# Kernel optimization log

Measured on AMD Instinct MI355X. Metric: run time of the kernel, lower is better.

## Reference

```python
import jax, jax.numpy as jnp
import numpy as np

H, SK, SV, PK, PV = 12, 16, 16, 4, 8
SCALAR_DIM, PAIR_DIM = 384, 128
SIZES = [SK*H, SK*H, SV*H, PK*H*3, PK*H*3, PV*H*3]  # qkv split sizes
N_LOGITS = 3
SS = (N_LOGITS * SK) ** -0.5                 # scalar logit scale
PS = (N_LOGITS * PK * 4.5) ** -0.5           # point logit scale
PBS = N_LOGITS ** -0.5                       # pair bias scale
EPS = 1e-8


def setup_inputs() -> dict:
    key = jax.random.key(0)
    ks = jax.random.split(key, 16)
    b, n = 1, 768
    scalar_feats = jax.random.normal(ks[0], (b, n, SCALAR_DIM), jnp.float32)
    pair_feats = jax.random.normal(ks[1], (b, n, n, PAIR_DIM), jnp.float32)
    rotations = jax.random.normal(ks[2], (b, n, 3, 3), jnp.float32)
    translations = jax.random.normal(ks[3], (b, n, 3), jnp.float32)
    mask = jnp.ones((b, n), dtype=bool)
    d_qkv = sum(SIZES)
    sc = SCALAR_DIM ** -0.5
    Wqkv = jax.random.normal(ks[4], (SCALAR_DIM, d_qkv), jnp.float32) * sc
    Wpb = jax.random.normal(ks[5], (PAIR_DIM, H), jnp.float32) * PAIR_DIM ** -0.5
    point_weights = jnp.full((1, H, 1, 1), float(np.log(np.e - 1.0)), jnp.float32)
    dim_out = H * (PAIR_DIM + SV + 4 * PV)  # 2112
    Wout = jax.random.normal(ks[6], (dim_out, SCALAR_DIM), jnp.float32) * dim_out ** -0.5
    bout = jnp.zeros((SCALAR_DIM,), jnp.float32)
    Wp1 = jax.random.normal(ks[7], (3 * H, PAIR_DIM), jnp.float32) * (3 * H) ** -0.5
    bp1 = jnp.zeros((PAIR_DIM,), jnp.float32)
    Wp2 = jax.random.normal(ks[8], (PAIR_DIM, PAIR_DIM), jnp.float32) * PAIR_DIM ** -0.5
    bp2 = jnp.zeros((PAIR_DIM,), jnp.float32)
    return dict(scalar_feats=scalar_feats, pair_feats=pair_feats, rotations=rotations,
                translations=translations, mask=mask, Wqkv=Wqkv, Wpb=Wpb,
                point_weights=point_weights, Wout=Wout, bout=bout,
                Wp1=Wp1, bp1=bp1, Wp2=Wp2, bp2=bp2)


def _heads(x, b, n, d):
    # b n (h d) -> b h n d
    return x.reshape(b, n, H, d).transpose(0, 2, 1, 3)


def _merge(x):
    # b h n d -> b n (h d)
    b, h, n, d = x.shape
    return x.transpose(0, 2, 1, 3).reshape(b, n, h * d)


def ipa_forward(scalar_feats, pair_feats, rotations, translations, mask,
                Wqkv, Wpb, point_weights, Wout, bout, Wp1, bp1, Wp2, bp2):
    b, n, _ = scalar_feats.shape
    qkv = scalar_feats @ Wqkv
    offs = np.cumsum([0] + SIZES)
    qs, ks_, vs, qp, kp, vp = [qkv[..., offs[i]:offs[i + 1]] for i in range(6)]
    qs, ks_, vs = _heads(qs, b, n, SK), _heads(ks_, b, n, SK), _heads(vs, b, n, SV)

    def to_global_points(p, d):
        p = p.reshape(b, n, H * d, 3)                       # ... (d c) -> ... d c
        p = jnp.einsum('bixy,bidy->bidx', rotations, p) + translations[:, :, None, :]
        return p.reshape(b, n, H, d, 3).transpose(0, 2, 1, 3, 4)  # b h n d 3

    qp, kp = to_global_points(qp, PK), to_global_points(kp, PK)
    vp = to_global_points(vp, PV)

    scalar_logits = jnp.einsum('bhid,bhjd->bhij', qs, ks_)
    pair_bias = jnp.einsum('bijd,dh->bhij', pair_feats, Wpb)
    point_logits = jnp.einsum('bhidc,bhjdc->bhij', qp, kp) * jax.nn.softplus(point_weights)

    m2 = mask[:, None, :, None] & mask[:, None, None, :]    # b 1 i j
    neg = -jnp.finfo(scalar_logits.dtype).max
    scalar_logits = jnp.where(m2, scalar_logits, neg)
    point_logits = jnp.where(m2, point_logits, neg)
    pair_bias = jnp.where(m2, pair_bias, neg)

    attn = jax.nn.softmax(SS * scalar_logits + PS * point_logits + PBS * pair_bias, axis=-1)

    res_scalar = jnp.einsum('bhij,bhjd->bhid', attn, vs)
    res_pair = jnp.einsum('bhij,bijd->bhid', attn, pair_feats)
    res_pts = jnp.einsum('bhij,bhjdc->bhidc', attn, vp)
    # inverse rigid: R^T (p - t)
    local = jnp.einsum('biyx,bhidy->bhidx', rotations,
                       res_pts - translations[:, None, :, None, :])
    pts_norm = jnp.sqrt(jnp.sum(local ** 2, axis=-1) + EPS)  # safe_norm

    feats = jnp.concatenate([
        _merge(res_scalar),                                   # b n h*SV
        _merge(res_pair),                                     # b n h*PAIR_DIM
        _merge(local.reshape(b, H, n, PV * 3)),               # b n h*PV*3
        _merge(pts_norm),                                     # b n h*PV
    ], axis=-1)
    scalar_out = feats @ Wout + bout

    edge = jnp.concatenate([attn,
                            jax.nn.softmax(point_logits, axis=-1),
                            jax.nn.softmax(scalar_logits, axis=-1)], axis=1)
    edge = edge.transpose(0, 2, 3, 1)                         # b i j (3h)
    pair_out = jax.nn.gelu(edge @ Wp1 + bp1, approximate=False) @ Wp2 + bp2
    return scalar_out, pair_out


def reference(scalar_feats, pair_feats, rotations, translations, mask,
              Wqkv, Wpb, point_weights, Wout, bout, Wp1, bp1, Wp2, bp2):
    return ipa_forward(scalar_feats, pair_feats, rotations, translations, mask,
                       Wqkv, Wpb, point_weights, Wout, bout, Wp1, bp1, Wp2, bp2)
```

## Files before the change

### kernel.cpp

```cpp
#include <hip/hip_runtime.h>
#include <hip/hip_bf16.h>
#include <math.h>

#define NRES 768
#define NH 12
#define DQKV 1152
#define PAIRD 128
#define SCD 384
#define DOUTF 2112

#define SS_C 0.14433756729740643f
#define PS_C 0.13608276348795434f
#define PBS_C 0.5773502691896258f

typedef __attribute__((ext_vector_type(4))) float f32x4;
typedef __attribute__((ext_vector_type(8))) short s16x8;

__device__ __forceinline__ unsigned short f2bf(float x) {
  union { float f; unsigned u; } v; v.f = x;
  unsigned r = (v.u + 0x7fffu + ((v.u >> 16) & 1u)) >> 16;
  return (unsigned short)r;
}
__device__ __forceinline__ float bf2f(unsigned short h) {
  union { unsigned u; float f; } v; v.u = (unsigned)h << 16;
  return v.f;
}

__device__ __forceinline__ float gelu_f(float x) {
  float z = x * 0.70710678118654752f;
  float az = fabsf(z);
  float t = __builtin_amdgcn_rcpf(1.f + 0.3275911f * az);
  float poly = t * (0.254829592f + t * (-0.284496736f +
               t * (1.421413741f + t * (-1.453152027f + t * 1.061405429f))));
  float e = __expf(-az * az);
  float erfv = 1.f - poly * e;
  erfv = (z < 0.f) ? -erfv : erfv;
  return 0.5f * x * (1.f + erfv);
}

__global__ __launch_bounds__(256) void gemm_bf16(
    const unsigned short* __restrict__ A, const unsigned short* __restrict__ Bt,
    const float* __restrict__ bias, float* __restrict__ C,
    int M, int Nn, int K)
{
  __shared__ __align__(16) unsigned short A_lds[64][72];
  __shared__ __align__(16) unsigned short B_lds[64][72];
  int m0 = blockIdx.y * 64, n0 = blockIdx.x * 64;
  int t = threadIdx.x;
  int lane = t & 63, w = t >> 6;
  int n15 = lane & 15, q = lane >> 4;
  f32x4 acc[4];
#pragma unroll
  for (int nt = 0; nt < 4; ++nt) acc[nt] = (f32x4){0.f, 0.f, 0.f, 0.f};
  for (int k0 = 0; k0 < K; k0 += 64) {
    __syncthreads();
#pragma unroll
    for (int u = 0; u < 2; ++u) {
      int idx = t + u * 256;
      int r = idx >> 3, c = (idx & 7) * 8;
      *(s16x8*)&A_lds[r][c] = *(const s16x8*)&A[(size_t)(m0 + r) * K + k0 + c];
      *(s16x8*)&B_lds[r][c] = *(const s16x8*)&Bt[(size_t)(n0 + r) * K + k0 + c];
    }
    __syncthreads();
#pragma unroll
    for (int ks = 0; ks < 2; ++ks) {
      s16x8 af = *(const s16x8*)&A_lds[w * 16 + n15][ks * 32 + q * 8];
#pragma unroll
      for (int nt = 0; nt < 4; ++nt) {
        s16x8 bf = *(const s16x8*)&B_lds[nt * 16 + n15][ks * 32 + q * 8];
        acc[nt] = __builtin_amdgcn_mfma_f32_16x16x32_bf16(af, bf, acc[nt], 0, 0, 0);
      }
    }
  }
#pragma unroll
  for (int nt = 0; nt < 4; ++nt) {
    int n = n0 + nt * 16 + n15;
    float bv = bias ? bias[n] : 0.f;
#pragma unroll
    for (int r = 0; r < 4; ++r) {
      int m = m0 + w * 16 + q * 4 + r;
      C[(size_t)m * Nn + n] = acc[nt][r] + bv;
    }
  }
}

__global__ __launch_bounds__(256) void prep_wqkv_kernel(
    const float* __restrict__ W, unsigned short* __restrict__ Bt)
{
  __shared__ float tile[32][33];
  int k0 = blockIdx.x * 32, n0 = blockIdx.y * 32;
  int t = threadIdx.x;
  int x = t & 31, y = t >> 5;
#pragma unroll
  for (int r = 0; r < 32; r += 8)
    tile[y + r][x] = W[(size_t)(k0 + y + r) * DQKV + n0 + x];
  __syncthreads();
#pragma unroll
  for (int r = 0; r < 32; r += 8) {
    float v = tile[x][y + r];
    unsigned short hi = f2bf(v);
    unsigned short lo = f2bf(v - bf2f(hi));
    size_t nrow = (size_t)(n0 + y + r) * 1152;
    Bt[nrow + k0 + x]       = hi;
    Bt[nrow + 384 + k0 + x] = lo;
    Bt[nrow + 768 + k0 + x] = hi;
  }
}

__global__ __launch_bounds__(128) void prep_a_kernel(
    const float* __restrict__ A, unsigned short* __restrict__ Ap)
{
  int i = blockIdx.x, t = threadIdx.x;
#pragma unroll
  for (int p = 0; p < 3; ++p) {
    int c = t + p * 128;
    float v = A[(size_t)i * SCD + c];
    unsigned short hi = f2bf(v);
    unsigned short lo = f2bf(v - bf2f(hi));
    size_t row = (size_t)i * 1152;
    Ap[row + c]       = hi;
    Ap[row + 384 + c] = hi;
    Ap[row + 768 + c] = lo;
  }
}

__global__ __launch_bounds__(256) void wt_kernel(
    const float* __restrict__ W, unsigned short* __restrict__ Wt)
{
  __shared__ float tile[32][33];
  int k0 = blockIdx.x * 32, n0 = blockIdx.y * 32;
  int t = threadIdx.x;
  int x = t & 31, y = t >> 5;
#pragma unroll
  for (int r = 0; r < 32; r += 8)
    tile[y + r][x] = W[(size_t)(k0 + y + r) * SCD + n0 + x];
  __syncthreads();
#pragma unroll
  for (int r = 0; r < 32; r += 8)
    Wt[(size_t)(n0 + y + r) * DOUTF + k0 + x] = f2bf(tile[x][y + r]);
}

__global__ __launch_bounds__(192) void points_kernel(
    const float* __restrict__ qkv, const float* __restrict__ rot,
    const float* __restrict__ trans, float* __restrict__ QP,
    float* __restrict__ KP, float* __restrict__ VP, float* __restrict__ Kq)
{
  int i = blockIdx.x;
  int t = threadIdx.x;
  const float* R = rot + (size_t)i * 9;
  const float* T = trans + (size_t)i * 3;
  int base; float* outp;
  if (t < 48) { int h = t >> 2, d = t & 3; base = 576 + (h * 4 + d) * 3;
    outp = QP + ((size_t)h * NRES + i) * 12 + d * 3; }
  else if (t < 96) { int u = t - 48; int h = u >> 2, d = u & 3; base = 720 + (h * 4 + d) * 3;
    outp = KP + ((size_t)h * NRES + i) * 12 + d * 3; }
  else { int u = t - 96; int h = u >> 3, d = u & 7; base = 864 + (h * 8 + d) * 3;
    outp = VP + ((size_t)h * NRES + i) * 24 + d * 3; }
  const float* p = qkv + (size_t)i * DQKV + base;
  float p0 = p[0], p1 = p[1], p2 = p[2];
#pragma unroll
  for (int x = 0; x < 3; ++x)
    outp[x] = R[x * 3 + 0] * p0 + R[x * 3 + 1] * p1 + R[x * 3 + 2] * p2 + T[x];
  {
    int h = t >> 4, d = t & 15;
    Kq[((size_t)h * NRES + i) * 16 + d] = qkv[(size_t)i * DQKV + 192 + h * 16 + d];
  }
}

__global__ __launch_bounds__(256) void vt_kernel(
    const float* __restrict__ qkv, const float* __restrict__ VP,
    unsigned short* __restrict__ Vt)
{
  int b = blockIdx.x;
  int h = b / 48, o = b % 48;
  int t = threadIdx.x;
  for (int p = 0; p < 3; ++p) {
    int j = p * 256 + t;
    float v;
    if (o < 16) v = qkv[(size_t)j * DQKV + 384 + h * 16 + o];
    else if (o < 40) v = VP[((size_t)h * NRES + j) * 24 + (o - 16)];
    else v = 0.f;
    Vt[((size_t)h * 48 + o) * NRES + j] = f2bf(v);
  }
}

__global__ __launch_bounds__(256) void pair_bias_kernel(
    const float* __restrict__ pair, const float* __restrict__ Wpb,
    float* __restrict__ Lb, unsigned short* __restrict__ pair_bT)
{
  __shared__ __align__(16) unsigned short Bt[64][136];
  int jt = blockIdx.x, i = blockIdx.y;
  int j0 = jt * 64;
  int t = threadIdx.x;
  int lane = t & 63, w = t >> 6;
  int n15 = lane & 15, q = lane >> 4;
  s16x8 wf[4];
#pragma unroll
  for (int ks = 0; ks < 4; ++ks) {
#pragma unroll
    for (int jj = 0; jj < 8; ++jj) {
      int k = ks * 32 + q * 8 + jj;
      float v = (n15 < 12) ? Wpb[k * 12 + n15] : 0.f;
      wf[ks][jj] = (short)f2bf(v);
    }
  }
  {
    int dq = t & 31, jb = t >> 5;
    for (int p = 0; p < 8; ++p) {
      int j = p * 8 + jb;
      float4 v = *(const float4*)(pair + ((size_t)i * NRES + j0 + j) * PAIRD + dq * 4);
      unsigned lo = (unsigned)f2bf(v.x) | ((unsigned)f2bf(v.y) << 16);
      unsigned hi = (unsigned)f2bf(v.z) | ((unsigned)f2bf(v.w) << 16);
      uint2 pk; pk.x = lo; pk.y = hi;
      *(uint2*)&Bt[j][dq * 4] = pk;
    }
  }
  __syncthreads();
  f32x4 acc = {0.f, 0.f, 0.f, 0.f};
  int m = w * 16 + n15;
#pragma unroll
  for (int ks = 0; ks < 4; ++ks) {
    s16x8 af = *(const s16x8*)&Bt[m][ks * 32 + q * 8];
    acc = __builtin_amdgcn_mfma_f32_16x16x32_bf16(af, wf[ks], acc, 0, 0, 0);
  }
  if (n15 < 12) {
    int j = j0 + w * 16 + q * 4;
    float4 st; st.x = acc[0]; st.y = acc[1]; st.z = acc[2]; st.w = acc[3];
    *(float4*)(Lb + ((size_t)n15 * NRES + i) * NRES + j) = st;
  }
  {
    int d = t >> 1, jh = t & 1;
#pragma unroll
    for (int c = 0; c < 4; ++c) {
      s16x8 pk;
#pragma unroll
      for (int e = 0; e < 8; ++e)
        pk[e] = (short)Bt[jh * 32 + c * 8 + e][d];
      *(s16x8*)&pair_bT[((size_t)i * PAIRD + d) * NRES + j0 + jh * 32 + c * 8] = pk;
    }
  }
}

#define RL 4
__global__ __launch_bounds__(256) void logits_softmax_kernel(
    const float* __restrict__ qkv, const float* __restrict__ Kq,
    const float* __restrict__ QP, const float* __restrict__ KP,
    const float* __restrict__ pw, const float* __restrict__ Lb,
    unsigned short* __restrict__ attn_b, unsigned short* __restrict__ sp_b,
    unsigned short* __restrict__ ss_b)
{
  int it = blockIdx.x, h = blockIdx.y;
  int i0 = it * RL;
  int t = threadIdx.x;
  __shared__ float q_sh[RL][28];
  if (t < RL * 28) {
    int r = t / 28, c = t % 28;
    q_sh[r][c] = (c < 16) ? qkv[(size_t)(i0 + r) * DQKV + h * 16 + c]
                          : QP[((size_t)h * NRES + i0 + r) * 12 + (c - 16)];
  }
  __syncthreads();
  float spw = log1pf(expf(pw[h]));
  float s[RL][3], p[RL][3], c[RL][3];
#pragma unroll
  for (int e = 0; e < 3; ++e) {
    int j = t + e * 256;
    float kr[16];
    const float* kq = Kq + ((size_t)h * NRES + j) * 16;
    *(float4*)&kr[0]  = *(const float4*)(kq + 0);
    *(float4*)&kr[4]  = *(const float4*)(kq + 4);
    *(float4*)&kr[8]  = *(const float4*)(kq + 8);
    *(float4*)&kr[12] = *(const float4*)(kq + 12);
    float kp[12];
    const float* kpp = KP + ((size_t)h * NRES + j) * 12;
    *(float4*)&kp[0] = *(const float4*)(kpp + 0);
    *(float4*)&kp[4] = *(const float4*)(kpp + 4);
    *(float4*)&kp[8] = *(const float4*)(kpp + 8);
#pragma unroll
    for (int r = 0; r < RL; ++r) {
      float sv = 0.f;
#pragma unroll
      for (int d = 0; d < 16; ++d) sv += q_sh[r][d] * kr[d];
      float pv = 0.f;
#pragma unroll
      for (int d = 0; d < 12; ++d) pv += q_sh[r][16 + d] * kp[d];
      pv *= spw;
      float bv = Lb[((size_t)h * NRES + i0 + r) * NRES + j];
      s[r][e] = sv; p[r][e] = pv;
      c[r][e] = SS_C * sv + PS_C * pv + PBS_C * bv;
    }
  }
  __shared__ float redm[4][RL][3];
  __shared__ float redsu[4][RL][3];
  int wv = t >> 6;
#pragma unroll
  for (int r = 0; r < RL; ++r) {
    float ms = fmaxf(fmaxf(s[r][0], s[r][1]), s[r][2]);
    float mp = fmaxf(fmaxf(p[r][0], p[r][1]), p[r][2]);
    float mc = fmaxf(fmaxf(c[r][0], c[r][1]), c[r][2]);
#pragma unroll
    for (int o = 32; o > 0; o >>= 1) {
      ms = fmaxf(ms, __shfl_down(ms, o));
      mp = fmaxf(mp, __shfl_down(mp, o));
      mc = fmaxf(mc, __shfl_down(mc, o));
    }
    if ((t & 63) == 0) { redm[wv][r][0] = ms; redm[wv][r][1] = mp; redm[wv][r][2] = mc; }
  }
  __syncthreads();
  float Ms[RL], Mp[RL], Mc[RL];
#pragma unroll
  for (int r = 0; r < RL; ++r) {
    Ms[r] = fmaxf(fmaxf(redm[0][r][0], redm[1][r][0]), fmaxf(redm[2][r][0], redm[3][r][0]));
    Mp[r] = fmaxf(fmaxf(redm[0][r][1], redm[1][r][1]), fmaxf(redm[2][r][1], redm[3][r][1]));
    Mc[r] = fmaxf(fmaxf(redm[0][r][2], redm[1][r][2]), fmaxf(redm[2][r][2], redm[3][r][2]));
  }
#pragma unroll
  for (int r = 0; r < RL; ++r) {
    float sums = 0.f, sump = 0.f, sumc = 0.f;
#pragma unroll
    for (int e = 0; e < 3; ++e) {
      float es = __expf(s[r][e] - Ms[r]); s[r][e] = es; sums += es;
      float ep = __expf(p[r][e] - Mp[r]); p[r][e] = ep; sump += ep;
      float ec = __expf(c[r][e] - Mc[r]); c[r][e] = ec; sumc += ec;
    }
#pragma unroll
    for (int o = 32; o > 0; o >>= 1) {
      sums += __shfl_down(sums, o);
      sump += __shfl_down(sump, o);
      sumc += __shfl_down(sumc, o);
    }
    if ((t & 63) == 0) { redsu[wv][r][0] = sums; redsu[wv][r][1] = sump; redsu[wv][r][2] = sumc; }
  }
  __syncthreads();
#pragma unroll
  for (int r = 0; r < RL; ++r) {
    float rs = 1.f / (redsu[0][r][0] + redsu[1][r][0] + redsu[2][r][0] + redsu[3][r][0]);
    float rp = 1.f / (redsu[0][r][1] + redsu[1][r][1] + redsu[2][r][1] + redsu[3][r][1]);
    float rc = 1.f / (redsu[0][r][2] + redsu[1][r][2] + redsu[2][r][2] + redsu[3][r][2]);
    size_t off = ((size_t)h * NRES + i0 + r) * NRES;
#pragma unroll
    for (int e = 0; e < 3; ++e) {
      int j = t + e * 256;
      ss_b[off + j]   = f2bf(s[r][e] * rs);
      sp_b[off + j]   = f2bf(p[r][e] * rp);
      attn_b[off + j] = f2bf(c[r][e] * rc);
    }
  }
}

__global__ __launch_bounds__(192) void res_sv_kernel(
    const unsigned short* __restrict__ attn, const unsigned short* __restrict__ Vt,
    float* __restrict__ res_sv)
{
  __shared__ __align__(16) unsigned short A_lds[16][72];
  __shared__ __align__(16) unsigned short B_lds[48][72];
  int it = blockIdx.x, h = blockIdx.y;
  int i0 = it * 16;
  int t = threadIdx.x;
  int lane = t & 63, w = t >> 6;
  int n15 = lane & 15, q = lane >> 4;
  f32x4 acc = {0.f, 0.f, 0.f, 0.f};
  for (int jt = 0; jt < 12; ++jt) {
    int j0 = jt * 64;
    __syncthreads();
    for (int idx = t; idx < 512; idx += 192) {
      int r = idx >> 5, j2 = idx & 31;
      *(unsigned*)&A_lds[r][j2 * 2] =
          *(const unsigned*)&attn[((size_t)h * NRES + i0 + r) * NRES + j0 + j2 * 2];
    }
    for (int idx = t; idx < 1536; idx += 192) {
      int o = idx >> 5, j2 = idx & 31;
      *(unsigned*)&B_lds[o][j2 * 2] =
          *(const unsigned*)&Vt[((size_t)h * 48 + o) * NRES + j0 + j2 * 2];
    }
    __syncthreads();
#pragma unroll
    for (int ks = 0; ks < 2; ++ks) {
      s16x8 af = *(const s16x8*)&A_lds[n15][ks * 32 + q * 8];
      s16x8 bf = *(const s16x8*)&B_lds[w * 16 + n15][ks * 32 + q * 8];
      acc = __builtin_amdgcn_mfma_f32_16x16x32_bf16(af, bf, acc, 0, 0, 0);
    }
  }
  int o = w * 16 + n15;
  if (o < 40) {
#pragma unroll
    for (int r = 0; r < 4; ++r) {
      int i = i0 + q * 4 + r;
      res_sv[((size_t)h * NRES + i) * 40 + o] = acc[r];
    }
  }
}

__global__ __launch_bounds__(256) void res_pair_kernel(
    const unsigned short* __restrict__ attn, const unsigned short* __restrict__ pair_bT,
    float* __restrict__ res_pair)
{
  __shared__ __align__(16) unsigned short A_lds[16][72];
  __shared__ __align__(16) unsigned short B_lds[128][72];
  int i = blockIdx.x;
  int t = threadIdx.x;
  int lane = t & 63, w = t >> 6;
  int n15 = lane & 15, q = lane >> 4;
  for (int idx = t; idx < 4 * 72; idx += 256)
    A_lds[12 + idx / 72][idx % 72] = 0;
  f32x4 acc[2];
  acc[0] = (f32x4){0.f, 0.f, 0.f, 0.f};
  acc[1] = (f32x4){0.f, 0.f, 0.f, 0.f};
  for (int jt = 0; jt < 12; ++jt) {
    int j0 = jt * 64;
    __syncthreads();
    for (int idx = t; idx < 384; idx += 256) {
      int r = idx >> 5, j2 = idx & 31;
      *(unsigned*)&A_lds[r][j2 * 2] =
          *(const unsigned*)&attn[((size_t)r * NRES + i) * NRES + j0 + j2 * 2];
    }
#pragma unroll
    for (int p = 0; p < 4; ++p) {
      int chunk = t + p * 256;
      int d = chunk >> 3, jc = (chunk & 7) * 8;
      *(s16x8*)&B_lds[d][jc] =
          *(const s16x8*)&pair_bT[((size_t)i * PAIRD + d) * NRES + j0 + jc];
    }
    __syncthreads();
#pragma unroll
    for (int ks = 0; ks < 2; ++ks) {
      s16x8 af = *(const s16x8*)&A_lds[n15][ks * 32 + q * 8];
#pragma unroll
      for (int nt = 0; nt < 2; ++nt) {
        int o = (w * 2 + nt) * 16 + n15;
        s16x8 bf = *(const s16x8*)&B_lds[o][ks * 32 + q * 8];
        acc[nt] = __builtin_amdgcn_mfma_f32_16x16x32_bf16(af, bf, acc[nt], 0, 0, 0);
      }
    }
  }
#pragma unroll
  for (int nt = 0; nt < 2; ++nt) {
    int o = (w * 2 + nt) * 16 + n15;
#pragma unroll
    for (int r = 0; r < 4; ++r) {
      int hh = q * 4 + r;
      if (hh < 12)
        res_pair[((size_t)hh * NRES + i) * PAIRD + o] = acc[nt][r];
    }
  }
}

__global__ __launch_bounds__(256) void feats_kernel(
    const float* __restrict__ res_sv, const float* __restrict__ res_pair,
    const float* __restrict__ rot, const float* __restrict__ trans,
    unsigned short* __restrict__ feats)
{
  int i = blockIdx.x;
  int t = threadIdx.x;
  unsigned short* F = feats + (size_t)i * DOUTF;
  if (t < 192) {
    int h = t >> 4, d = t & 15;
    F[t] = f2bf(res_sv[((size_t)h * NRES + i) * 40 + d]);
  }
  for (int e = 0; e < 6; ++e) {
    int idx = e * 256 + t;
    int h = idx >> 7, o = idx & 127;
    F[192 + idx] = f2bf(res_pair[((size_t)h * NRES + i) * PAIRD + o]);
  }
  if (t < 96) {
    int h = t >> 3, d = t & 7;
    const float* R = rot + (size_t)i * 9;
    const float* T = trans + (size_t)i * 3;
    const float* pp = res_sv + ((size_t)h * NRES + i) * 40 + 16 + d * 3;
    float p0 = pp[0] - T[0], p1 = pp[1] - T[1], p2 = pp[2] - T[2];
    float l0 = R[0] * p0 + R[3] * p1 + R[6] * p2;
    float l1 = R[1] * p0 + R[4] * p1 + R[7] * p2;
    float l2 = R[2] * p0 + R[5] * p1 + R[8] * p2;
    F[1728 + h * 24 + d * 3 + 0] = f2bf(l0);
    F[1728 + h * 24 + d * 3 + 1] = f2bf(l1);
    F[1728 + h * 24 + d * 3 + 2] = f2bf(l2);
    F[2016 + h * 8 + d] = f2bf(sqrtf(l0 * l0 + l1 * l1 + l2 * l2 + 1e-8f));
  }
}

__global__ __launch_bounds__(256) void mlp_kernel(
    const unsigned short* __restrict__ attn, const unsigned short* __restrict__ sp,
    const unsigned short* __restrict__ ss, const float* __restrict__ Wp1,
    const float* __restrict__ bp1, const float* __restrict__ Wp2,
    const float* __restrict__ bp2, float* __restrict__ out)
{
  __shared__ __align__(16) unsigned short E_lds[2][64][72];
  __shared__ __align__(16) unsigned short A_lds[64][136];
  int t = threadIdx.x;
  int lane = t & 63, w = t >> 6;
  int n15 = lane & 15, q = lane >> 4;
  for (int idx = t; idx < 64 * 28 * 2; idx += 256) {
    int b = idx / (64 * 28);
    int r = (idx / 28) % 64, k = 36 + idx % 28;
    E_lds[b][r][k] = 0;
  }
  s16x8 w1f[2][2], w2f[4][2];
#pragma unroll
  for (int ks = 0; ks < 2; ++ks)
#pragma unroll
    for (int nt = 0; nt < 2; ++nt) {
      int nn = (w * 2 + nt) * 16 + n15;
#pragma unroll
      for (int jj = 0; jj < 8; ++jj) {
        int k = ks * 32 + q * 8 + jj;
        w1f[ks][nt][jj] = (k < 36) ? (short)f2bf(Wp1[(size_t)k * 128 + nn]) : (short)0;
      }
    }
#pragma unroll
  for (int ks = 0; ks < 4; ++ks)
#pragma unroll
    for (int nt = 0; nt < 2; ++nt) {
      int nn = (w * 2 + nt) * 16 + n15;
#pragma unroll
      for (int jj = 0; jj < 8; ++jj) {
        int k = ks * 32 + q * 8 + jj;
        w2f[ks][nt][jj] = (short)f2bf(Wp2[(size_t)k * 128 + nn]);
      }
    }
  float b1v[2], b2v[2];
#pragma unroll
  for (int nt = 0; nt < 2; ++nt) {
    int nn = (w * 2 + nt) * 16 + n15;
    b1v[nt] = bp1[nn];
    b2v[nt] = bp2[nn];
  }
  const unsigned short* bufs[3] = {attn, sp, ss};
  const int NT = NRES * 12;
  int ej = t & 63, ecb = t >> 6;
  int tile = blockIdx.x;
  int cur = 0;
  if (tile < NT) {
    int i = tile / 12, j0 = (tile % 12) * 64;
#pragma unroll
    for (int p = 0; p < 9; ++p) {
      int cc = ecb * 9 + p;
      E_lds[0][ej][cc] = bufs[cc / 12][((size_t)(cc % 12) * NRES + i) * NRES + j0 + ej];
    }
  }
  for (; tile < NT; tile += gridDim.x) {
    int nxt = tile + gridDim.x;
    __syncthreads();
    unsigned short ev[9];
    if (nxt < NT) {
      int i2 = nxt / 12, j02 = (nxt % 12) * 64;
#pragma unroll
      for (int p = 0; p < 9; ++p) {
        int cc = ecb * 9 + p;
        ev[p] = bufs[cc / 12][((size_t)(cc % 12) * NRES + i2) * NRES + j02 + ej];
      }
    }
    f32x4 c1[4][2];
#pragma unroll
    for (int mt = 0; mt < 4; ++mt) {
#pragma unroll
      for (int nt = 0; nt < 2; ++nt) c1[mt][nt] = (f32x4){0.f, 0.f, 0.f, 0.f};
#pragma unroll
      for (int ks = 0; ks < 2; ++ks) {
        s16x8 af = *(const s16x8*)&E_lds[cur][mt * 16 + n15][ks * 32 + q * 8];
#pragma unroll
        for (int nt = 0; nt < 2; ++nt)
          c1[mt][nt] = __builtin_amdgcn_mfma_f32_16x16x32_bf16(af, w1f[ks][nt], c1[mt][nt], 0, 0, 0);
      }
    }
#pragma unroll
    for (int mt = 0; mt < 4; ++mt)
#pragma unroll
      for (int nt = 0; nt < 2; ++nt) {
        int o = (w * 2 + nt) * 16 + n15;
#pragma unroll
        for (int r = 0; r < 4; ++r) {
          float x = c1[mt][nt][r] + b1v[nt];
          A_lds[mt * 16 + q * 4 + r][o] = f2bf(gelu_f(x));
        }
      }
    if (nxt < NT) {
#pragma unroll
      for (int p = 0; p < 9; ++p)
        E_lds[cur ^ 1][ej][ecb * 9 + p] = ev[p];
    }
    __syncthreads();
    int i = tile / 12, j0 = (tile % 12) * 64;
    f32x4 c2[4][2];
#pragma unroll
    for (int mt = 0; mt < 4; ++mt) {
#pragma unroll
      for (int nt = 0; nt < 2; ++nt) c2[mt][nt] = (f32x4){0.f, 0.f, 0.f, 0.f};
#pragma unroll
      for (int ks = 0; ks < 4; ++ks) {
        s16x8 af = *(const s16x8*)&A_lds[mt * 16 + n15][ks * 32 + q * 8];
#pragma unroll
        for (int nt = 0; nt < 2; ++nt)
          c2[mt][nt] = __builtin_amdgcn_mfma_f32_16x16x32_bf16(af, w2f[ks][nt], c2[mt][nt], 0, 0, 0);
      }
    }
#pragma unroll
    for (int mt = 0; mt < 4; ++mt)
#pragma unroll
      for (int nt = 0; nt < 2; ++nt) {
        int o = (w * 2 + nt) * 16 + n15;
        int jb = j0 + mt * 16 + q * 4;
#pragma unroll
        for (int r = 0; r < 4; ++r)
          out[((size_t)i * NRES + jb + r) * PAIRD + o] = c2[mt][nt][r] + b2v[nt];
      }
    cur ^= 1;
  }
}

extern "C" void kernel_launch(void* const* d_in, const int* in_sizes, int n_in,
                              void* d_out, int out_size, void* d_ws, size_t ws_size,
                              hipStream_t stream) {
  const float* scalar_feats = (const float*)d_in[0];
  const float* pair  = (const float*)d_in[1];
  const float* rot   = (const float*)d_in[2];
  const float* trans = (const float*)d_in[3];
  const float* Wqkv  = (const float*)d_in[5];
  const float* Wpb   = (const float*)d_in[6];
  const float* pw    = (const float*)d_in[7];
  const float* Wout  = (const float*)d_in[8];
  const float* bout  = (const float*)d_in[9];
  const float* Wp1   = (const float*)d_in[10];
  const float* bp1   = (const float*)d_in[11];
  const float* Wp2   = (const float*)d_in[12];
  const float* bp2   = (const float*)d_in[13];
  float* out = (float*)d_out;
  float* ws = (float*)d_ws;

  float* qkv = ws;
  float* QP  = ws + 884736;
  float* KP  = ws + 995328;
  float* VP  = ws + 1105920;
  unsigned short* Vt = (unsigned short*)(ws + 1327104);
  float* Lb  = ws + 1548288;
  unsigned short* attn_b = (unsigned short*)(ws + 8626176);
  unsigned short* sp_b   = (unsigned short*)(ws + 12165120);
  unsigned short* ss_b   = (unsigned short*)(ws + 15704064);
  float* res_sv   = ws + 19243008;
  float* res_pair = ws + 19611648;
  unsigned short* feats_b = (unsigned short*)(ws + 20791296);
  unsigned short* Wout_t  = (unsigned short*)(ws + 21602304);
  float* Kq = ws + 22007808;
  unsigned short* Aprime  = (unsigned short*)(ws + 22155264);
  unsigned short* Wqkv_t  = (unsigned short*)(ws + 22597632);
  unsigned short* pair_bT = (unsigned short*)(ws + 23261184);

  prep_wqkv_kernel<<<dim3(SCD / 32, DQKV / 32), 256, 0, stream>>>(Wqkv, Wqkv_t);
  prep_a_kernel<<<NRES, 128, 0, stream>>>(scalar_feats, Aprime);
  gemm_bf16<<<dim3(DQKV / 64, NRES / 64), 256, 0, stream>>>(
      Aprime, Wqkv_t, nullptr, qkv, NRES, DQKV, 1152);
  points_kernel<<<NRES, 192, 0, stream>>>(qkv, rot, trans, QP, KP, VP, Kq);
  vt_kernel<<<576, 256, 0, stream>>>(qkv, VP, Vt);
  pair_bias_kernel<<<dim3(12, NRES), 256, 0, stream>>>(pair, Wpb, Lb, pair_bT);
  logits_softmax_kernel<<<dim3(NRES / RL, 12), 256, 0, stream>>>(
      qkv, Kq, QP, KP, pw, Lb, attn_b, sp_b, ss_b);
  res_sv_kernel<<<dim3(48, 12), 192, 0, stream>>>(attn_b, Vt, res_sv);
  res_pair_kernel<<<NRES, 256, 0, stream>>>(attn_b, pair_bT, res_pair);
  feats_kernel<<<NRES, 256, 0, stream>>>(res_sv, res_pair, rot, trans, feats_b);
  wt_kernel<<<dim3(DOUTF / 32, SCD / 32), 256, 0, stream>>>(Wout, Wout_t);
  gemm_bf16<<<dim3(SCD / 64, NRES / 64), 256, 0, stream>>>(
      feats_b, Wout_t, bout, out, NRES, SCD, DOUTF);
  mlp_kernel<<<2304, 256, 0, stream>>>(attn_b, sp_b, ss_b, Wp1, bp1, Wp2, bp2, out + 294912);
}
```

Measured before the change: 872.1 us.

## Restructure pair MLP so each wave owns a 16-row tile, removing block barriers

```diff
diff --git a/kernel.cpp b/kernel.cpp
--- a/kernel.cpp
+++ b/kernel.cpp
@@ -483,126 +483,106 @@
     const float* __restrict__ bp1, const float* __restrict__ Wp2,
     const float* __restrict__ bp2, float* __restrict__ out)
 {
-  __shared__ __align__(16) unsigned short E_lds[2][64][72];
-  __shared__ __align__(16) unsigned short A_lds[64][136];
+  __shared__ __align__(16) unsigned short W1T[128][72];
+  __shared__ __align__(16) unsigned short W2T[128][136];
+  __shared__ __align__(16) unsigned short E_w[4][16][72];
+  __shared__ __align__(16) unsigned short A_w[4][16][136];
   int t = threadIdx.x;
   int lane = t & 63, w = t >> 6;
   int n15 = lane & 15, q = lane >> 4;
-  for (int idx = t; idx < 64 * 28 * 2; idx += 256) {
-    int b = idx / (64 * 28);
-    int r = (idx / 28) % 64, k = 36 + idx % 28;
-    E_lds[b][r][k] = 0;
-  }
-  s16x8 w1f[2][2], w2f[4][2];
-#pragma unroll
-  for (int ks = 0; ks < 2; ++ks)
-#pragma unroll
-    for (int nt = 0; nt < 2; ++nt) {
-      int nn = (w * 2 + nt) * 16 + n15;
-#pragma unroll
-      for (int jj = 0; jj < 8; ++jj) {
-        int k = ks * 32 + q * 8 + jj;
-        w1f[ks][nt][jj] = (k < 36) ? (short)f2bf(Wp1[(size_t)k * 128 + nn]) : (short)0;
-      }
-    }
-#pragma unroll
-  for (int ks = 0; ks < 4; ++ks)
-#pragma unroll
-    for (int nt = 0; nt < 2; ++nt) {
-      int nn = (w * 2 + nt) * 16 + n15;
-#pragma unroll
-      for (int jj = 0; jj < 8; ++jj) {
-        int k = ks * 32 + q * 8 + jj;
-        w2f[ks][nt][jj] = (short)f2bf(Wp2[(size_t)k * 128 + nn]);
-      }
-    }
-  float b1v[2], b2v[2];
-#pragma unroll
-  for (int nt = 0; nt < 2; ++nt) {
-    int nn = (w * 2 + nt) * 16 + n15;
-    b1v[nt] = bp1[nn];
-    b2v[nt] = bp2[nn];
-  }
+  for (int idx = t; idx < 128 * 64; idx += 256) {
+    int o = idx & 127, k = idx >> 7;
+    W1T[o][k] = (k < 36) ? f2bf(Wp1[(size_t)k * 128 + o]) : 0;
+  }
+  for (int idx = t; idx < 128 * 128; idx += 256) {
+    int o = idx & 127, k = idx >> 7;
+    W2T[o][k] = f2bf(Wp2[(size_t)k * 128 + o]);
+  }
+  for (int idx = lane; idx < 16 * 28; idx += 64) {
+    int j = idx / 28, k = 36 + idx % 28;
+    E_w[w][j][k] = 0;
+  }
+  float b1v[8], b2v[8];
+#pragma unroll
+  for (int nt = 0; nt < 8; ++nt) {
+    b1v[nt] = bp1[nt * 16 + n15];
+    b2v[nt] = bp2[nt * 16 + n15];
+  }
+  __syncthreads();
   const unsigned short* bufs[3] = {attn, sp, ss};
-  const int NT = NRES * 12;
-  int ej = t & 63, ecb = t >> 6;
-  int tile = blockIdx.x;
-  int cur = 0;
-  if (tile < NT) {
-    int i = tile / 12, j0 = (tile % 12) * 64;
+  const int NT = NRES * 48;
+  const int step = gridDim.x * 4;
+  int g = blockIdx.x * 4 + w;
+  if (g < NT) {
+    int i = g / 48, j0 = (g % 48) * 16;
 #pragma unroll
     for (int p = 0; p < 9; ++p) {
-      int cc = ecb * 9 + p;
-      E_lds[0][ej][cc] = bufs[cc / 12][((size_t)(cc % 12) * NRES + i) * NRES + j0 + ej];
-    }
-  }
-  for (; tile < NT; tile += gridDim.x) {
-    int nxt = tile + gridDim.x;
-    __syncthreads();
+      int idx = p * 64 + lane;
+      int c = idx >> 4, j = idx & 15;
+      E_w[w][j][c] = bufs[c / 12][((size_t)(c % 12) * NRES + i) * NRES + j0 + j];
+    }
+  }
+  for (; g < NT; g += step) {
+    int i = g / 48, j0 = (g % 48) * 16;
+    int g2 = g + step;
+    f32x4 c1[8];
+#pragma unroll
+    for (int nt = 0; nt < 8; ++nt) c1[nt] = (f32x4){0.f, 0.f, 0.f, 0.f};
+#pragma unroll
+    for (int ks = 0; ks < 2; ++ks) {
+      s16x8 af = *(const s16x8*)&E_w[w][n15][ks * 32 + q * 8];
+#pragma unroll
+      for (int nt = 0; nt < 8; ++nt) {
+        s16x8 bf = *(const s16x8*)&W1T[nt * 16 + n15][ks * 32 + q * 8];
+        c1[nt] = __builtin_amdgcn_mfma_f32_16x16x32_bf16(af, bf, c1[nt], 0, 0, 0);
+      }
+    }
     unsigned short ev[9];
-    if (nxt < NT) {
-      int i2 = nxt / 12, j02 = (nxt % 12) * 64;
+    if (g2 < NT) {
+      int i2 = g2 / 48, j02 = (g2 % 48) * 16;
 #pragma unroll
       for (int p = 0; p < 9; ++p) {
-        int cc = ecb * 9 + p;
-        ev[p] = bufs[cc / 12][((size_t)(cc % 12) * NRES + i2) * NRES + j02 + ej];
-      }
-    }
-    f32x4 c1[4][2];
-#pragma unroll
-    for (int mt = 0; mt < 4; ++mt) {
-#pragma unroll
-      for (int nt = 0; nt < 2; ++nt) c1[mt][nt] = (f32x4){0.f, 0.f, 0.f, 0.f};
-#pragma unroll
-      for (int ks = 0; ks < 2; ++ks) {
-        s16x8 af = *(const s16x8*)&E_lds[cur][mt * 16 + n15][ks * 32 + q * 8];
-#pragma unroll
-        for (int nt = 0; nt < 2; ++nt)
-          c1[mt][nt] = __builtin_amdgcn_mfma_f32_16x16x32_bf16(af, w1f[ks][nt], c1[mt][nt], 0, 0, 0);
-      }
-    }
-#pragma unroll
-    for (int mt = 0; mt < 4; ++mt)
-#pragma unroll
-      for (int nt = 0; nt < 2; ++nt) {
-        int o = (w * 2 + nt) * 16 + n15;
-#pragma unroll
-        for (int r = 0; r < 4; ++r) {
-          float x = c1[mt][nt][r] + b1v[nt];
-          A_lds[mt * 16 + q * 4 + r][o] = f2bf(gelu_f(x));
-        }
-      }
-    if (nxt < NT) {
-#pragma unroll
-      for (int p = 0; p < 9; ++p)
-        E_lds[cur ^ 1][ej][ecb * 9 + p] = ev[p];
-    }
-    __syncthreads();
-    int i = tile / 12, j0 = (tile % 12) * 64;
-    f32x4 c2[4][2];
-#pragma unroll
-    for (int mt = 0; mt < 4; ++mt) {
-#pragma unroll
-      for (int nt = 0; nt < 2; ++nt) c2[mt][nt] = (f32x4){0.f, 0.f, 0.f, 0.f};
-#pragma unroll
-      for (int ks = 0; ks < 4; ++ks) {
-        s16x8 af = *(const s16x8*)&A_lds[mt * 16 + n15][ks * 32 + q * 8];
-#pragma unroll
-        for (int nt = 0; nt < 2; ++nt)
-          c2[mt][nt] = __builtin_amdgcn_mfma_f32_16x16x32_bf16(af, w2f[ks][nt], c2[mt][nt], 0, 0, 0);
-      }
-    }
-#pragma unroll
-    for (int mt = 0; mt < 4; ++mt)
-#pragma unroll
-      for (int nt = 0; nt < 2; ++nt) {
-        int o = (w * 2 + nt) * 16 + n15;
-        int jb = j0 + mt * 16 + q * 4;
-#pragma unroll
-        for (int r = 0; r < 4; ++r)
-          out[((size_t)i * NRES + jb + r) * PAIRD + o] = c2[mt][nt][r] + b2v[nt];
-      }
-    cur ^= 1;
+        int idx = p * 64 + lane;
+        int c = idx >> 4, j = idx & 15;
+        ev[p] = bufs[c / 12][((size_t)(c % 12) * NRES + i2) * NRES + j02 + j];
+      }
+    }
+#pragma unroll
+    for (int nt = 0; nt < 8; ++nt)
+#pragma unroll
+      for (int r = 0; r < 4; ++r) {
+        float x = c1[nt][r] + b1v[nt];
+        A_w[w][q * 4 + r][nt * 16 + n15] = f2bf(gelu_f(x));
+      }
+    f32x4 c2[8];
+#pragma unroll
+    for (int nt = 0; nt < 8; ++nt) c2[nt] = (f32x4){0.f, 0.f, 0.f, 0.f};
+#pragma unroll
+    for (int ks = 0; ks < 4; ++ks) {
+      s16x8 af = *(const s16x8*)&A_w[w][n15][ks * 32 + q * 8];
+#pragma unroll
+      for (int nt = 0; nt < 8; ++nt) {
+        s16x8 bf = *(const s16x8*)&W2T[nt * 16 + n15][ks * 32 + q * 8];
+        c2[nt] = __builtin_amdgcn_mfma_f32_16x16x32_bf16(af, bf, c2[nt], 0, 0, 0);
+      }
+    }
+    if (g2 < NT) {
+#pragma unroll
+      for (int p = 0; p < 9; ++p) {
+        int idx = p * 64 + lane;
+        int c = idx >> 4, j = idx & 15;
+        E_w[w][j][c] = ev[p];
+      }
+    }
+#pragma unroll
+    for (int nt = 0; nt < 8; ++nt) {
+      int o = nt * 16 + n15;
+#pragma unroll
+      for (int r = 0; r < 4; ++r) {
+        int jb = j0 + q * 4 + r;
+        out[((size_t)i * NRES + jb) * PAIRD + o] = c2[nt][r] + b2v[nt];
+      }
+    }
   }
 }
 
```

Measured after the change: 885.5 us. About the same (+1.5%).

## Software-pipeline pair MLP: overlap layer-2 of previous tile with layer-1

Applied to the files above, without the earlier changes.

```diff
diff --git a/kernel.cpp b/kernel.cpp
--- a/kernel.cpp
+++ b/kernel.cpp
@@ -484,7 +484,7 @@
     const float* __restrict__ bp2, float* __restrict__ out)
 {
   __shared__ __align__(16) unsigned short E_lds[2][64][72];
-  __shared__ __align__(16) unsigned short A_lds[64][136];
+  __shared__ __align__(16) unsigned short A_lds[2][64][136];
   int t = threadIdx.x;
   int lane = t & 63, w = t >> 6;
   int n15 = lane & 15, q = lane >> 4;
@@ -528,6 +528,7 @@
   int ej = t & 63, ecb = t >> 6;
   int tile = blockIdx.x;
   int cur = 0;
+  int prevTile = -1;
   if (tile < NT) {
     int i = tile / 12, j0 = (tile % 12) * 64;
 #pragma unroll
@@ -536,9 +537,9 @@
       E_lds[0][ej][cc] = bufs[cc / 12][((size_t)(cc % 12) * NRES + i) * NRES + j0 + ej];
     }
   }
+  __syncthreads();
   for (; tile < NT; tile += gridDim.x) {
     int nxt = tile + gridDim.x;
-    __syncthreads();
     unsigned short ev[9];
     if (nxt < NT) {
       int i2 = nxt / 12, j02 = (nxt % 12) * 64;
@@ -561,6 +562,32 @@
           c1[mt][nt] = __builtin_amdgcn_mfma_f32_16x16x32_bf16(af, w1f[ks][nt], c1[mt][nt], 0, 0, 0);
       }
     }
+    if (prevTile >= 0) {
+      f32x4 c2[4][2];
+#pragma unroll
+      for (int mt = 0; mt < 4; ++mt) {
+#pragma unroll
+        for (int nt = 0; nt < 2; ++nt) c2[mt][nt] = (f32x4){0.f, 0.f, 0.f, 0.f};
+#pragma unroll
+        for (int ks = 0; ks < 4; ++ks) {
+          s16x8 af = *(const s16x8*)&A_lds[cur ^ 1][mt * 16 + n15][ks * 32 + q * 8];
+#pragma unroll
+          for (int nt = 0; nt < 2; ++nt)
+            c2[mt][nt] = __builtin_amdgcn_mfma_f32_16x16x32_bf16(af, w2f[ks][nt], c2[mt][nt], 0, 0, 0);
+        }
+      }
+      int ip = prevTile / 12, j0p = (prevTile % 12) * 64;
+#pragma unroll
+      for (int mt = 0; mt < 4; ++mt)
+#pragma unroll
+        for (int nt = 0; nt < 2; ++nt) {
+          int o = (w * 2 + nt) * 16 + n15;
+          int jb = j0p + mt * 16 + q * 4;
+#pragma unroll
+          for (int r = 0; r < 4; ++r)
+            out[((size_t)ip * NRES + jb + r) * PAIRD + o] = c2[mt][nt][r] + b2v[nt];
+        }
+    }
 #pragma unroll
     for (int mt = 0; mt < 4; ++mt)
 #pragma unroll
@@ -569,7 +596,7 @@
 #pragma unroll
         for (int r = 0; r < 4; ++r) {
           float x = c1[mt][nt][r] + b1v[nt];
-          A_lds[mt * 16 + q * 4 + r][o] = f2bf(gelu_f(x));
+          A_lds[cur][mt * 16 + q * 4 + r][o] = f2bf(gelu_f(x));
         }
       }
     if (nxt < NT) {
@@ -578,7 +605,10 @@
         E_lds[cur ^ 1][ej][ecb * 9 + p] = ev[p];
     }
     __syncthreads();
-    int i = tile / 12, j0 = (tile % 12) * 64;
+    prevTile = tile;
+    cur ^= 1;
+  }
+  if (prevTile >= 0) {
     f32x4 c2[4][2];
 #pragma unroll
     for (int mt = 0; mt < 4; ++mt) {
@@ -586,23 +616,23 @@
       for (int nt = 0; nt < 2; ++nt) c2[mt][nt] = (f32x4){0.f, 0.f, 0.f, 0.f};
 #pragma unroll
       for (int ks = 0; ks < 4; ++ks) {
-        s16x8 af = *(const s16x8*)&A_lds[mt * 16 + n15][ks * 32 + q * 8];
+        s16x8 af = *(const s16x8*)&A_lds[cur ^ 1][mt * 16 + n15][ks * 32 + q * 8];
 #pragma unroll
         for (int nt = 0; nt < 2; ++nt)
           c2[mt][nt] = __builtin_amdgcn_mfma_f32_16x16x32_bf16(af, w2f[ks][nt], c2[mt][nt], 0, 0, 0);
       }
     }
+    int ip = prevTile / 12, j0p = (prevTile % 12) * 64;
 #pragma unroll
     for (int mt = 0; mt < 4; ++mt)
 #pragma unroll
       for (int nt = 0; nt < 2; ++nt) {
         int o = (w * 2 + nt) * 16 + n15;
-        int jb = j0 + mt * 16 + q * 4;
+        int jb = j0p + mt * 16 + q * 4;
 #pragma unroll
         for (int r = 0; r < 4; ++r)
-          out[((size_t)i * NRES + jb + r) * PAIRD + o] = c2[mt][nt][r] + b2v[nt];
-      }
-    cur ^= 1;
+          out[((size_t)ip * NRES + jb + r) * PAIRD + o] = c2[mt][nt][r] + b2v[nt];
+      }
   }
 }
 
```

New measurement: 867.9 us. Within noise of the previous version (-0.5%).
